# Performance work log

Measured on AMD Instinct MI355X. Metric: run time of the kernel, lower is better.

The kernel has to match this reference:

```python
import jax, jax.numpy as jnp
import numpy as np

N_HEAD = 8


def _axial_attn(x, wq, wk, wv, fw, fb, axis):
    # x: (B, T, H, W, C); axis is the axial axis in (B, nh, T, H, W, d): 2=T, 3=H, 4=W
    B, T, H, W, C = x.shape
    d = C // N_HEAD

    def heads(y):
        # (B,T,H,W,C) -> (B, nh, T, H, W, d)
        return jnp.moveaxis(y.reshape(B, T, H, W, N_HEAD, d), -2, 1)

    q, k, v = heads(x @ wq), heads(x @ wk), heads(x @ wv)
    # restrict attention to the axial axis: move it to -2, all other dims are batch
    q = jnp.moveaxis(q, axis, -2)
    k = jnp.moveaxis(k, axis, -2)
    v = jnp.moveaxis(v, axis, -2)
    scale = 1.0 / jnp.sqrt(jnp.asarray(d, x.dtype))
    scores = jnp.einsum('...ld,...md->...lm', q * scale, k)
    att = jax.nn.softmax(scores, axis=-1)
    o = jnp.einsum('...lm,...md->...ld', att, v)
    o = jnp.moveaxis(o, -2, axis)            # restore axial axis position
    o = jnp.moveaxis(o, 1, -2).reshape(B, T, H, W, C)  # merge heads
    return o @ fw + fb


def setup_inputs() -> dict:
    key = jax.random.key(0)
    ks = jax.random.split(key, 16)
    C = 512
    x = jax.random.normal(ks[0], (4, C, 16, 32, 32), jnp.float32)
    s = 0.02

    def w(k):
        return jax.random.normal(k, (C, C), jnp.float32) * s

    inp = {'x': x}
    i = 1
    for ax in ('w', 'h', 't'):
        inp[f'wq_{ax}'] = w(ks[i])
        inp[f'wk_{ax}'] = w(ks[i + 1])
        inp[f'wv_{ax}'] = w(ks[i + 2])
        inp[f'fc_{ax}'] = w(ks[i + 3])
        inp[f'fb_{ax}'] = jnp.zeros((C,), jnp.float32)
        i += 4
    return inp


def reference(x, wq_w, wk_w, wv_w, fc_w, fb_w,
              wq_h, wk_h, wv_h, fc_h, fb_h,
              wq_t, wk_t, wv_t, fc_t, fb_t):
    xt = jnp.moveaxis(x, 1, -1)  # (B, C, T, H, W) -> (B, T, H, W, C)
    out = (_axial_attn(xt, wq_w, wk_w, wv_w, fc_w, fb_w, 4)   # attend along W
           + _axial_attn(xt, wq_h, wk_h, wv_h, fc_h, fb_h, 3)  # attend along H
           + _axial_attn(xt, wq_t, wk_t, wv_t, fc_t, fb_t, 2))  # attend along T
    return jnp.moveaxis(out, -1, 1)  # back to (B, C, T, H, W)
```

## Files before the change

kernel.cpp:

```cpp
#include <hip/hip_runtime.h>
#include <stdint.h>

typedef __attribute__((ext_vector_type(8))) short bf16x8;
typedef __attribute__((ext_vector_type(4))) float f32x4;

static __device__ __forceinline__ short f2bf(float f) {
  uint32_t u = __builtin_bit_cast(uint32_t, f);
  u += 0x7fffu + ((u >> 16) & 1u);
  return (short)(u >> 16);
}

static __device__ __forceinline__ void gload_lds16(const void* g, void* l) {
  __builtin_amdgcn_global_load_lds((const __attribute__((address_space(1))) void*)g,
                                   (__attribute__((address_space(3))) void*)l, 16, 0, 0);
}

#define GFENCE asm volatile("" ::: "memory")

__global__ __launch_bounds__(256) void transpose_x_k(const float* __restrict__ x,
                                                     short* __restrict__ xb) {
  __shared__ float t[64][65];
  const int pt = blockIdx.x, ct = blockIdx.y, b = blockIdx.z;
  const int tid = threadIdx.x;
#pragma unroll
  for (int i = 0; i < 16; i++) {
    int cc = i * 4 + (tid >> 6);
    int pp = tid & 63;
    t[cc][pp] = x[(size_t)(b * 512 + ct * 64 + cc) * 16384 + pt * 64 + pp];
  }
  __syncthreads();
#pragma unroll
  for (int i = 0; i < 2; i++) {
    int seg = i * 256 + tid;
    int pw = seg >> 3, c8 = seg & 7;
    short tmp[8];
#pragma unroll
    for (int k = 0; k < 8; k++) tmp[k] = f2bf(t[c8 * 8 + k][pw]);
    *(uint4*)&xb[(size_t)(b * 16384 + pt * 64 + pw) * 512 + ct * 64 + c8 * 8] =
        *(const uint4*)tmp;
  }
}

struct WPtrs {
  const float* src[12];
  short* dst[12];
  int ld[12];
};

__global__ __launch_bounds__(256) void transpose_w_k(WPtrs P) {
  __shared__ float t[64][65];
  const int kt = blockIdx.x, nt = blockIdx.y, z = blockIdx.z;
  const float* src = P.src[z];
  short* dst = P.dst[z];
  const int ld = P.ld[z];
  const int tid = threadIdx.x;
#pragma unroll
  for (int i = 0; i < 16; i++) {
    int kk = i * 4 + (tid >> 6);
    int nn = tid & 63;
    t[kk][nn] = src[(kt * 64 + kk) * 512 + nt * 64 + nn];
  }
  __syncthreads();
#pragma unroll
  for (int i = 0; i < 2; i++) {
    int seg = i * 256 + tid;
    int nn = seg >> 3, k8 = seg & 7;
    short tmp[8];
#pragma unroll
    for (int k = 0; k < 8; k++) tmp[k] = f2bf(t[k8 * 8 + k][nn]);
    *(uint4*)&dst[(size_t)(nt * 64 + nn) * ld + kt * 64 + k8 * 8] = *(const uint4*)tmp;
  }
}

__global__ void bsum_k(const float* a, const float* b, const float* c, float* o) {
  int i = blockIdx.x * 256 + threadIdx.x;
  if (i < 512) o[i] = a[i] + b[i] + c[i];
}

#define LOADB(b, kh)                                                           \
  do {                                                                         \
    _Pragma("unroll") for (int ni = 0; ni < 4; ++ni) bfr[ni] =                 \
        *(const bf16x8*)(smem + ((b) * 4 + 2 + (kh)) * 16384 + boff +          \
                         ni * 1024);                                           \
  } while (0)

#define LOADA(b, kh, mq)                                                       \
  do {                                                                         \
    _Pragma("unroll") for (int mi = 0; mi < 4; ++mi) af[mi] =                  \
        *(const bf16x8*)(smem + ((b) * 4 + (kh)) * 16384 + aoff +              \
                         ((mq) * 4 + mi) * 1024);                              \
  } while (0)

#define MFMA16(mq)                                                             \
  do {                                                                         \
    __builtin_amdgcn_s_setprio(1);                                             \
    _Pragma("unroll") for (int mi = 0; mi < 4; ++mi)                           \
        _Pragma("unroll") for (int ni = 0; ni < 4; ++ni) acc[(mq) * 4 + mi]    \
            [ni] = __builtin_amdgcn_mfma_f32_16x16x32_bf16(                    \
                af[mi], bfr[ni], acc[(mq) * 4 + mi][ni], 0, 0, 0);             \
    __builtin_amdgcn_s_setprio(0);                                             \
    GFENCE;                                                                    \
  } while (0)

#define TILE(b, W0, W2, S0, S1, S2, S3)                                        \
  do {                                                                         \
    asm volatile("s_waitcnt vmcnt(" W0 ")" ::: "memory");                      \
    __builtin_amdgcn_s_barrier();                                              \
    GFENCE;                                                                    \
    LOADB(b, 0);                                                               \
    LOADA(b, 0, 0);                                                            \
    S0;                                                                        \
    MFMA16(0);                                                                 \
    __builtin_amdgcn_s_barrier();                                              \
    GFENCE;                                                                    \
    LOADA(b, 0, 1);                                                            \
    S1;                                                                        \
    MFMA16(1);                                                                 \
    asm volatile("s_waitcnt vmcnt(" W2 ")" ::: "memory");                      \
    __builtin_amdgcn_s_barrier();                                              \
    GFENCE;                                                                    \
    LOADB(b, 1);                                                               \
    LOADA(b, 1, 0);                                                            \
    S2;                                                                        \
    MFMA16(0);                                                                 \
    __builtin_amdgcn_s_barrier();                                              \
    GFENCE;                                                                    \
    LOADA(b, 1, 1);                                                            \
    S3;                                                                        \
    MFMA16(1);                                                                 \
  } while (0)

template <int MODE>
__global__ __launch_bounds__(512, 2) void gemm256_k(const short* __restrict__ A,
                                                    int lda,
                                                    const short* __restrict__ B,
                                                    int ldb, void* __restrict__ Dp,
                                                    int K, int ldd,
                                                    const float* __restrict__ bsum,
                                                    int GN) {
  extern __shared__ char smem[];
  const int tid = threadIdx.x;
  const int lane = tid & 63, wave = tid >> 6;
  const int wr = wave >> 2, wc = wave & 3;
  const int r4 = lane & 15, kl = lane >> 4;

  int bid = blockIdx.x;
  const int cpx = gridDim.x >> 3;
  bid = (bid & 7) * cpx + (bid >> 3);
  int bm, bn;
  if constexpr (MODE == 0) {
    bn = bid % GN;
    bm = bid / GN;
  } else {
    bm = bid & 1;
    bn = bid >> 1;
  }

  const int NT = K >> 6;

  const int srow = tid >> 2;
  const int schk = (tid & 3) ^ ((tid >> 4) & 3);
  const short* gA0 = A + (size_t)(bm * 256 + srow) * lda + schk * 8;
  const short* gB0 = B + (size_t)(bn * 256 + srow) * ldb + schk * 8;

  auto stage = [&](int tt, int x) {
    const short* g = (x < 2) ? gA0 : gB0;
    const size_t rstep = (size_t)128 * ((x < 2) ? lda : ldb);
    const size_t koff = (size_t)tt * 64 + (x & 1) * 32;
    char* ldst = smem + (((tt & 1) * 4 + x) * 16384) + wave * 1024;
#pragma unroll
    for (int i = 0; i < 2; ++i)
      gload_lds16(g + i * rstep + koff, ldst + i * 8192);
  };

  const int kls = kl ^ (r4 >> 2);
  const int aoff = wr * 8192 + r4 * 64 + kls * 16;
  const int boff = wc * 4096 + r4 * 64 + kls * 16;

  f32x4 acc[8][4];
#pragma unroll
  for (int i = 0; i < 8; ++i)
#pragma unroll
    for (int j = 0; j < 4; ++j) acc[i][j] = (f32x4){0.f, 0.f, 0.f, 0.f};
  bf16x8 af[4], bfr[4];

  stage(0, 0);
  stage(0, 2);
  stage(0, 1);
  stage(0, 3);
  stage(1, 0);
  stage(1, 2);

  int t = 0;
  for (; t < NT - 2; ++t) {
    const int b = t & 1;
    TILE(b, "8", "8", stage(t + 1, 1), stage(t + 1, 3), stage(t + 2, 0),
         stage(t + 2, 2));
  }
  {
    const int b = t & 1;
    TILE(b, "8", "8", stage(t + 1, 1), stage(t + 1, 3), (void)0, (void)0);
    ++t;
  }
  {
    const int b = t & 1;
    TILE(b, "4", "0", (void)0, (void)0, (void)0, (void)0);
  }

  const int m0 = wr * 128 + kl * 4;
  const int n0 = wc * 64 + r4;
  if (MODE == 0) {
    short* D = (short*)Dp;
#pragma unroll
    for (int mi = 0; mi < 8; ++mi)
#pragma unroll
      for (int ni = 0; ni < 4; ++ni)
#pragma unroll
        for (int r = 0; r < 4; ++r) {
          int row = bm * 256 + m0 + mi * 16 + r;
          int col = bn * 256 + n0 + ni * 16;
          D[(size_t)row * ldd + col] = f2bf(acc[mi][ni][r]);
        }
  } else {
    float* D = (float*)Dp + (size_t)((bn * 256) >> 14) * 8388608;
#pragma unroll
    for (int mi = 0; mi < 8; ++mi)
#pragma unroll
      for (int ni = 0; ni < 4; ++ni)
#pragma unroll
        for (int r = 0; r < 4; ++r) {
          int c = bm * 256 + m0 + mi * 16 + r;
          int n = (bn * 256 + n0 + ni * 16) & 16383;
          if (MODE == 1)
            D[(size_t)c * 16384 + n] = acc[mi][ni][r] + bsum[c];
          else
            D[(size_t)c * 16384 + n] += acc[mi][ni][r];
        }
  }
}

template <int L>
__global__ __launch_bounds__(256) void attn_mfma_k(const short* __restrict__ qkv,
                                                   short* __restrict__ o, int Adiv,
                                                   int Bmul, int Cmul, int stride,
                                                   int obase) {
  constexpr int MT = L / 16;
  constexpr int PITCH = 40;
  __shared__ short lds[4 * (32 + 64) * PITCH];
  const int tid = threadIdx.x;
  const int lane = tid & 63, wave = tid >> 6;
  short* p_lds = lds + wave * (96 * PITCH);
  short* vt = p_lds + 32 * PITCH;

  const int wid = blockIdx.x * 4 + wave;
  const int s = wid >> 3, head = wid & 7;
  const int base = (s / Adiv) * Bmul + (s % Adiv) * Cmul;
  const int r4 = lane & 15, kl = lane >> 4;

  if constexpr (L == 16) {
    for (int i = lane; i < 96 * PITCH; i += 64) p_lds[i] = 0;
  }

  bf16x8 qf[MT][2], kf[MT][2];
#pragma unroll
  for (int mi = 0; mi < MT; ++mi)
#pragma unroll
    for (int ks = 0; ks < 2; ++ks) {
      size_t nrow = (size_t)(base + (mi * 16 + r4) * stride) * 1536 + head * 64 +
                    ks * 32 + kl * 8;
      qf[mi][ks] = *(const bf16x8*)&qkv[nrow];
      kf[mi][ks] = *(const bf16x8*)&qkv[nrow + 512];
    }

#pragma unroll
  for (int it = 0; it < L / 8; ++it) {
    int j = (lane >> 3) + it * 8;
    uint4 u = *(const uint4*)&qkv[(size_t)(base + j * stride) * 1536 + 1024 +
                                  head * 64 + (lane & 7) * 8];
    ushort e[8];
    *(uint4*)e = u;
#pragma unroll
    for (int q = 0; q < 8; ++q) vt[((lane & 7) * 8 + q) * PITCH + j] = (short)e[q];
  }

  f32x4 sacc[MT][MT];
#pragma unroll
  for (int i = 0; i < MT; ++i)
#pragma unroll
    for (int j = 0; j < MT; ++j) sacc[i][j] = (f32x4){0.f, 0.f, 0.f, 0.f};
#pragma unroll
  for (int mi = 0; mi < MT; ++mi)
#pragma unroll
    for (int ni = 0; ni < MT; ++ni)
#pragma unroll
      for (int ks = 0; ks < 2; ++ks)
        sacc[mi][ni] = __builtin_amdgcn_mfma_f32_16x16x32_bf16(
            qf[mi][ks], kf[ni][ks], sacc[mi][ni], 0, 0, 0);

#pragma unroll
  for (int mi = 0; mi < MT; ++mi) {
    float mx[4], sm[4];
#pragma unroll
    for (int r = 0; r < 4; ++r) {
      float m = sacc[mi][0][r];
      if (MT == 2) m = fmaxf(m, sacc[mi][1][r]);
#pragma unroll
      for (int d = 1; d < 16; d <<= 1) m = fmaxf(m, __shfl_xor(m, d));
      mx[r] = m;
    }
#pragma unroll
    for (int ni = 0; ni < MT; ++ni)
#pragma unroll
      for (int r = 0; r < 4; ++r)
        sacc[mi][ni][r] = __expf((sacc[mi][ni][r] - mx[r]) * 0.125f);
#pragma unroll
    for (int r = 0; r < 4; ++r) {
      float t = sacc[mi][0][r];
      if (MT == 2) t += sacc[mi][1][r];
#pragma unroll
      for (int d = 1; d < 16; d <<= 1) t += __shfl_xor(t, d);
      sm[r] = 1.0f / t;
    }
#pragma unroll
    for (int ni = 0; ni < MT; ++ni)
#pragma unroll
      for (int r = 0; r < 4; ++r)
        p_lds[(mi * 16 + kl * 4 + r) * PITCH + ni * 16 + r4] =
            f2bf(sacc[mi][ni][r] * sm[r]);
  }
  asm volatile("s_waitcnt lgkmcnt(0)" ::: "memory");

  bf16x8 paf[MT], vbf[4];
#pragma unroll
  for (int mi = 0; mi < MT; ++mi)
    paf[mi] = *(const bf16x8*)&p_lds[(mi * 16 + r4) * PITCH + kl * 8];
#pragma unroll
  for (int nd = 0; nd < 4; ++nd)
    vbf[nd] = *(const bf16x8*)&vt[(nd * 16 + r4) * PITCH + kl * 8];
  f32x4 oacc[MT][4];
#pragma unroll
  for (int i = 0; i < MT; ++i)
#pragma unroll
    for (int j = 0; j < 4; ++j) oacc[i][j] = (f32x4){0.f, 0.f, 0.f, 0.f};
#pragma unroll
  for (int mi = 0; mi < MT; ++mi)
#pragma unroll
    for (int nd = 0; nd < 4; ++nd)
      oacc[mi][nd] = __builtin_amdgcn_mfma_f32_16x16x32_bf16(paf[mi], vbf[nd],
                                                             oacc[mi][nd], 0, 0, 0);

#pragma unroll
  for (int mi = 0; mi < MT; ++mi)
#pragma unroll
    for (int r = 0; r < 4; ++r) {
      int n = base + (mi * 16 + kl * 4 + r) * stride;
      size_t ob = (size_t)n * 1536 + obase + head * 64 + r4;
#pragma unroll
      for (int nd = 0; nd < 4; ++nd) o[ob + nd * 16] = f2bf(oacc[mi][nd][r]);
    }
}

extern "C" void kernel_launch(void* const* d_in, const int* in_sizes, int n_in,
                              void* d_out, int out_size, void* d_ws, size_t ws_size,
                              hipStream_t stream) {
  const float* x = (const float*)d_in[0];
  const float* wq[3];
  const float* wk[3];
  const float* wv[3];
  const float* fc[3];
  const float* fb[3];
  for (int a = 0; a < 3; a++) {
    wq[a] = (const float*)d_in[1 + a * 5];
    wk[a] = (const float*)d_in[2 + a * 5];
    wv[a] = (const float*)d_in[3 + a * 5];
    fc[a] = (const float*)d_in[4 + a * 5];
    fb[a] = (const float*)d_in[5 + a * 5];
  }
  char* ws = (char*)d_ws;
  short* xb = (short*)(ws);
  short* qkv = (short*)(ws + 67108864);
  short* wqkvt = (short*)(ws + 268435456);
  short* fctA = (short*)(ws + 273154048);
  float* bsum = (float*)(ws + 274726912);
  short* ob = (short*)(ws + 274728960);
  float* out = (float*)d_out;

  (void)hipFuncSetAttribute((const void*)&gemm256_k<0>,
                            hipFuncAttributeMaxDynamicSharedMemorySize, 131072);
  (void)hipFuncSetAttribute((const void*)&gemm256_k<1>,
                            hipFuncAttributeMaxDynamicSharedMemorySize, 131072);

  WPtrs P;
  for (int a = 0; a < 3; a++) {
    P.src[a * 4 + 0] = wq[a];
    P.src[a * 4 + 1] = wk[a];
    P.src[a * 4 + 2] = wv[a];
    P.src[a * 4 + 3] = fc[a];
    P.dst[a * 4 + 0] = wqkvt + (size_t)a * 1536 * 512;
    P.dst[a * 4 + 1] = wqkvt + (size_t)a * 1536 * 512 + 512 * 512;
    P.dst[a * 4 + 2] = wqkvt + (size_t)a * 1536 * 512 + 2 * 512 * 512;
    P.dst[a * 4 + 3] = fctA + a * 512;
    P.ld[a * 4 + 0] = 512;
    P.ld[a * 4 + 1] = 512;
    P.ld[a * 4 + 2] = 512;
    P.ld[a * 4 + 3] = 1536;
  }
  transpose_w_k<<<dim3(8, 8, 12), 256, 0, stream>>>(P);
  bsum_k<<<dim3(2), 256, 0, stream>>>(fb[0], fb[1], fb[2], bsum);
  transpose_x_k<<<dim3(256, 8, 4), 256, 0, stream>>>(x, xb);

  const int Ad[3] = {1, 32, 1024};
  const int Bm_[3] = {32, 1024, 16384};
  const int Cm[3] = {0, 1, 1};
  const int St[3] = {1, 32, 1024};
  const int Ls[3] = {32, 32, 16};

  for (int a = 0; a < 3; a++) {
    gemm256_k<0><<<dim3(1536), 512, 131072, stream>>>(
        xb, 512, wqkvt + (size_t)a * 1536 * 512, 512, (void*)qkv, 512, 1536,
        nullptr, 6);
    if (Ls[a] == 32)
      attn_mfma_k<32><<<dim3(4096), 256, 0, stream>>>(qkv, ob, Ad[a], Bm_[a], Cm[a],
                                                      St[a], a * 512);
    else
      attn_mfma_k<16><<<dim3(8192), 256, 0, stream>>>(qkv, ob, Ad[a], Bm_[a], Cm[a],
                                                      St[a], a * 512);
  }
  gemm256_k<1><<<dim3(512), 512, 131072, stream>>>(
      fctA, 1536, ob, 1536, (void*)out, 1536, 0, bsum, 0);
}
```

Baseline: 705.4 us.

## Double-buffer GEMM register fragments to prefetch LDS reads ahead of MFMAs

Rewrites the 256x256 bf16 GEMM main loop so the A/B fragments are held in two register sets. The LDS reads for the next quarter-tile, and for the next K tile's first fragments, are issued before the current MFMA batch runs. The aim is to hide LDS read latency behind matrix math, with vmcnt waits moved to fit the new order. This raises register pressure under the 512-thread, 2-blocks launch bound. The epilogue also drops the MODE 2 accumulate path, which changes results if that mode is still called.

After: 697.0 us. No clear change (-1.2%).

```diff
diff --git a/kernel.cpp b/kernel.cpp
--- a/kernel.cpp
+++ b/kernel.cpp
@@ -77,57 +77,64 @@
   if (i < 512) o[i] = a[i] + b[i] + c[i];
 }
 
-#define LOADB(b, kh)                                                           \
+#define READ_B(DST, b, kh)                                                     \
   do {                                                                         \
-    _Pragma("unroll") for (int ni = 0; ni < 4; ++ni) bfr[ni] =                 \
+    _Pragma("unroll") for (int ni = 0; ni < 4; ++ni) DST[ni] =                 \
         *(const bf16x8*)(smem + ((b) * 4 + 2 + (kh)) * 16384 + boff +          \
                          ni * 1024);                                           \
   } while (0)
 
-#define LOADA(b, kh, mq)                                                       \
+#define READ_A(DST, b, kh, mq)                                                 \
   do {                                                                         \
-    _Pragma("unroll") for (int mi = 0; mi < 4; ++mi) af[mi] =                  \
+    _Pragma("unroll") for (int mi = 0; mi < 4; ++mi) DST[mi] =                 \
         *(const bf16x8*)(smem + ((b) * 4 + (kh)) * 16384 + aoff +              \
                          ((mq) * 4 + mi) * 1024);                              \
   } while (0)
 
-#define MFMA16(mq)                                                             \
+#define MFMAX(mq, AF, BF)                                                      \
   do {                                                                         \
     __builtin_amdgcn_s_setprio(1);                                             \
     _Pragma("unroll") for (int mi = 0; mi < 4; ++mi)                           \
         _Pragma("unroll") for (int ni = 0; ni < 4; ++ni) acc[(mq) * 4 + mi]    \
             [ni] = __builtin_amdgcn_mfma_f32_16x16x32_bf16(                    \
-                af[mi], bfr[ni], acc[(mq) * 4 + mi][ni], 0, 0, 0);             \
+                AF[mi], BF[ni], acc[(mq) * 4 + mi][ni], 0, 0, 0);              \
     __builtin_amdgcn_s_setprio(0);                                             \
     GFENCE;                                                                    \
   } while (0)
 
-#define TILE(b, W0, W2, S0, S1, S2, S3)                                        \
+#define TILE_RA(b, b2, W1, W3, S0, S1, S2, S3, RA)                             \
   do {                                                                         \
-    asm volatile("s_waitcnt vmcnt(" W0 ")" ::: "memory");                      \
+                            \
     __builtin_amdgcn_s_barrier();                                              \
     GFENCE;                                                                    \
-    LOADB(b, 0);                                                               \
-    LOADA(b, 0, 0);                                                            \
+    READ_A(afB, b, 0, 1);                                                      \
     S0;                                                                        \
-    MFMA16(0);                                                                 \
+    GFENCE;                                                                    \
+    MFMAX(0, afA, bfA);                                                        \
+                     \
+    asm volatile("s_waitcnt vmcnt(" W1 ")" ::: "memory");                      \
     __builtin_amdgcn_s_barrier();                                              \
     GFENCE;                                                                    \
-    LOADA(b, 0, 1);                                                            \
+    READ_B(bfB, b, 1);                                                         \
+    READ_A(afA, b, 1, 0);                                                      \
     S1;                                                                        \
-    MFMA16(1);                                                                 \
-    asm volatile("s_waitcnt vmcnt(" W2 ")" ::: "memory");                      \
+    GFENCE;                                                                    \
+    MFMAX(1, afB, bfA);                                                        \
+                            \
     __builtin_amdgcn_s_barrier();                                              \
     GFENCE;                                                                    \
-    LOADB(b, 1);                                                               \
-    LOADA(b, 1, 0);                                                            \
+    READ_A(afB, b, 1, 1);                                                      \
     S2;                                                                        \
-    MFMA16(0);                                                                 \
+    GFENCE;                                                                    \
+    MFMAX(0, afA, bfB);                                                        \
+                 \
+    asm volatile("s_waitcnt vmcnt(" W3 ")" ::: "memory");                      \
     __builtin_amdgcn_s_barrier();                                              \
     GFENCE;                                                                    \
-    LOADA(b, 1, 1);                                                            \
+    RA;                                                                        \
     S3;                                                                        \
-    MFMA16(1);                                                                 \
+    GFENCE;                                                                    \
+    MFMAX(1, afB, bfB);                                                        \
   } while (0)
 
 template <int MODE>
@@ -182,7 +189,7 @@
   for (int i = 0; i < 8; ++i)
 #pragma unroll
     for (int j = 0; j < 4; ++j) acc[i][j] = (f32x4){0.f, 0.f, 0.f, 0.f};
-  bf16x8 af[4], bfr[4];
+  bf16x8 afA[4], afB[4], bfA[4], bfB[4];
 
   stage(0, 0);
   stage(0, 2);
@@ -190,21 +197,33 @@
   stage(0, 3);
   stage(1, 0);
   stage(1, 2);
+  asm volatile("s_waitcnt vmcnt(8)" ::: "memory");
+  __builtin_amdgcn_s_barrier();
+  GFENCE;
+  READ_B(bfA, 0, 0);
+  READ_A(afA, 0, 0, 0);
+  GFENCE;
 
   int t = 0;
   for (; t < NT - 2; ++t) {
-    const int b = t & 1;
-    TILE(b, "8", "8", stage(t + 1, 1), stage(t + 1, 3), stage(t + 2, 0),
-         stage(t + 2, 2));
+    const int b = t & 1, b2 = b ^ 1;
+    TILE_RA(b, b2, "6", "6", stage(t + 1, 1), stage(t + 1, 3), stage(t + 2, 0),
+            stage(t + 2, 2), {
+              READ_B(bfA, b2, 0);
+              READ_A(afA, b2, 0, 0);
+            });
   }
   {
-    const int b = t & 1;
-    TILE(b, "8", "8", stage(t + 1, 1), stage(t + 1, 3), (void)0, (void)0);
+    const int b = t & 1, b2 = b ^ 1;
+    TILE_RA(b, b2, "6", "4", stage(t + 1, 1), stage(t + 1, 3), (void)0, (void)0, {
+      READ_B(bfA, b2, 0);
+      READ_A(afA, b2, 0, 0);
+    });
     ++t;
   }
   {
-    const int b = t & 1;
-    TILE(b, "4", "0", (void)0, (void)0, (void)0, (void)0);
+    const int b = t & 1, b2 = b ^ 1;
+    TILE_RA(b, b2, "0", "0", (void)0, (void)0, (void)0, (void)0, (void)0);
   }
 
   const int m0 = wr * 128 + kl * 4;
@@ -231,10 +250,7 @@
         for (int r = 0; r < 4; ++r) {
           int c = bm * 256 + m0 + mi * 16 + r;
           int n = (bn * 256 + n0 + ni * 16) & 16383;
-          if (MODE == 1)
-            D[(size_t)c * 16384 + n] = acc[mi][ni][r] + bsum[c];
-          else
-            D[(size_t)c * 16384 + n] += acc[mi][ni][r];
+          D[(size_t)c * 16384 + n] = acc[mi][ni][r] + bsum[c];
         }
   }
 }
```

## Run 256x256 GEMM with 16 waves per block, one load per stage

Applied to the files above, without the earlier changes.

The GEMM block grows from 512 to 1024 threads, so each of 16 waves owns a 64x64 output sub-tile instead of 128x64. Per-thread accumulators halve and each stage issues a single global-to-LDS load per thread. The four-phase tile schedule with in-between barriers becomes two phases per k-tile, with adjusted vmcnt waits. This trades register pressure and per-wave MFMA work for more waves to hide latency, but adds barrier cost across 16 waves and lowers MFMA-to-LDS-read reuse per wave.

Measured after the change: 735.8 us. +4.3%, slower.

```diff
diff --git a/kernel.cpp b/kernel.cpp
--- a/kernel.cpp
+++ b/kernel.cpp
@@ -77,67 +77,46 @@
   if (i < 512) o[i] = a[i] + b[i] + c[i];
 }
 
-#define LOADB(b, kh)                                                           \
+#define READ_AB(b, kh)                                                         \
   do {                                                                         \
     _Pragma("unroll") for (int ni = 0; ni < 4; ++ni) bfr[ni] =                 \
         *(const bf16x8*)(smem + ((b) * 4 + 2 + (kh)) * 16384 + boff +          \
                          ni * 1024);                                           \
+    _Pragma("unroll") for (int mi = 0; mi < 4; ++mi) af[mi] =                  \
+        *(const bf16x8*)(smem + ((b) * 4 + (kh)) * 16384 + aoff + mi * 1024);  \
   } while (0)
 
-#define LOADA(b, kh, mq)                                                       \
-  do {                                                                         \
-    _Pragma("unroll") for (int mi = 0; mi < 4; ++mi) af[mi] =                  \
-        *(const bf16x8*)(smem + ((b) * 4 + (kh)) * 16384 + aoff +              \
-                         ((mq) * 4 + mi) * 1024);                              \
-  } while (0)
-
-#define MFMA16(mq)                                                             \
+#define MFMA16X                                                                \
   do {                                                                         \
     __builtin_amdgcn_s_setprio(1);                                             \
     _Pragma("unroll") for (int mi = 0; mi < 4; ++mi)                           \
-        _Pragma("unroll") for (int ni = 0; ni < 4; ++ni) acc[(mq) * 4 + mi]    \
-            [ni] = __builtin_amdgcn_mfma_f32_16x16x32_bf16(                    \
-                af[mi], bfr[ni], acc[(mq) * 4 + mi][ni], 0, 0, 0);             \
+        _Pragma("unroll") for (int ni = 0; ni < 4; ++ni) acc[mi][ni] =         \
+            __builtin_amdgcn_mfma_f32_16x16x32_bf16(af[mi], bfr[ni],           \
+                                                    acc[mi][ni], 0, 0, 0);     \
     __builtin_amdgcn_s_setprio(0);                                             \
     GFENCE;                                                                    \
   } while (0)
 
-#define TILE(b, W0, W2, S0, S1, S2, S3)                                        \
+#define PH(b, kh, W, SA, SB)                                                   \
   do {                                                                         \
-    asm volatile("s_waitcnt vmcnt(" W0 ")" ::: "memory");                      \
+    asm volatile("s_waitcnt vmcnt(" W ")" ::: "memory");                       \
     __builtin_amdgcn_s_barrier();                                              \
     GFENCE;                                                                    \
-    LOADB(b, 0);                                                               \
-    LOADA(b, 0, 0);                                                            \
-    S0;                                                                        \
-    MFMA16(0);                                                                 \
-    __builtin_amdgcn_s_barrier();                                              \
+    READ_AB(b, kh);                                                            \
+    SA;                                                                        \
+    SB;                                                                        \
     GFENCE;                                                                    \
-    LOADA(b, 0, 1);                                                            \
-    S1;                                                                        \
-    MFMA16(1);                                                                 \
-    asm volatile("s_waitcnt vmcnt(" W2 ")" ::: "memory");                      \
-    __builtin_amdgcn_s_barrier();                                              \
-    GFENCE;                                                                    \
-    LOADB(b, 1);                                                               \
-    LOADA(b, 1, 0);                                                            \
-    S2;                                                                        \
-    MFMA16(0);                                                                 \
-    __builtin_amdgcn_s_barrier();                                              \
-    GFENCE;                                                                    \
-    LOADA(b, 1, 1);                                                            \
-    S3;                                                                        \
-    MFMA16(1);                                                                 \
+    MFMA16X;                                                                   \
   } while (0)
 
 template <int MODE>
-__global__ __launch_bounds__(512, 2) void gemm256_k(const short* __restrict__ A,
-                                                    int lda,
-                                                    const short* __restrict__ B,
-                                                    int ldb, void* __restrict__ Dp,
-                                                    int K, int ldd,
-                                                    const float* __restrict__ bsum,
-                                                    int GN) {
+__global__ __launch_bounds__(1024) void gemm256_k(const short* __restrict__ A,
+                                                  int lda,
+                                                  const short* __restrict__ B,
+                                                  int ldb, void* __restrict__ Dp,
+                                                  int K, int ldd,
+                                                  const float* __restrict__ bsum,
+                                                  int GN) {
   extern __shared__ char smem[];
   const int tid = threadIdx.x;
   const int lane = tid & 63, wave = tid >> 6;
@@ -165,21 +144,17 @@
 
   auto stage = [&](int tt, int x) {
     const short* g = (x < 2) ? gA0 : gB0;
-    const size_t rstep = (size_t)128 * ((x < 2) ? lda : ldb);
     const size_t koff = (size_t)tt * 64 + (x & 1) * 32;
-    char* ldst = smem + (((tt & 1) * 4 + x) * 16384) + wave * 1024;
-#pragma unroll
-    for (int i = 0; i < 2; ++i)
-      gload_lds16(g + i * rstep + koff, ldst + i * 8192);
+    gload_lds16(g + koff, smem + (((tt & 1) * 4 + x) * 16384) + wave * 1024);
   };
 
   const int kls = kl ^ (r4 >> 2);
-  const int aoff = wr * 8192 + r4 * 64 + kls * 16;
+  const int aoff = wr * 4096 + r4 * 64 + kls * 16;
   const int boff = wc * 4096 + r4 * 64 + kls * 16;
 
-  f32x4 acc[8][4];
-#pragma unroll
-  for (int i = 0; i < 8; ++i)
+  f32x4 acc[4][4];
+#pragma unroll
+  for (int i = 0; i < 4; ++i)
 #pragma unroll
     for (int j = 0; j < 4; ++j) acc[i][j] = (f32x4){0.f, 0.f, 0.f, 0.f};
   bf16x8 af[4], bfr[4];
@@ -194,25 +169,27 @@
   int t = 0;
   for (; t < NT - 2; ++t) {
     const int b = t & 1;
-    TILE(b, "8", "8", stage(t + 1, 1), stage(t + 1, 3), stage(t + 2, 0),
-         stage(t + 2, 2));
+    PH(b, 0, "4", stage(t + 1, 1), stage(t + 1, 3));
+    PH(b, 1, "4", stage(t + 2, 0), stage(t + 2, 2));
   }
   {
     const int b = t & 1;
-    TILE(b, "8", "8", stage(t + 1, 1), stage(t + 1, 3), (void)0, (void)0);
+    PH(b, 0, "4", stage(t + 1, 1), stage(t + 1, 3));
+    PH(b, 1, "4", (void)0, (void)0);
     ++t;
   }
   {
     const int b = t & 1;
-    TILE(b, "4", "0", (void)0, (void)0, (void)0, (void)0);
-  }
-
-  const int m0 = wr * 128 + kl * 4;
+    PH(b, 0, "2", (void)0, (void)0);
+    PH(b, 1, "0", (void)0, (void)0);
+  }
+
+  const int m0 = wr * 64 + kl * 4;
   const int n0 = wc * 64 + r4;
   if (MODE == 0) {
     short* D = (short*)Dp;
 #pragma unroll
-    for (int mi = 0; mi < 8; ++mi)
+    for (int mi = 0; mi < 4; ++mi)
 #pragma unroll
       for (int ni = 0; ni < 4; ++ni)
 #pragma unroll
@@ -224,17 +201,14 @@
   } else {
     float* D = (float*)Dp + (size_t)((bn * 256) >> 14) * 8388608;
 #pragma unroll
-    for (int mi = 0; mi < 8; ++mi)
+    for (int mi = 0; mi < 4; ++mi)
 #pragma unroll
       for (int ni = 0; ni < 4; ++ni)
 #pragma unroll
         for (int r = 0; r < 4; ++r) {
           int c = bm * 256 + m0 + mi * 16 + r;
           int n = (bn * 256 + n0 + ni * 16) & 16383;
-          if (MODE == 1)
-            D[(size_t)c * 16384 + n] = acc[mi][ni][r] + bsum[c];
-          else
-            D[(size_t)c * 16384 + n] += acc[mi][ni][r];
+          D[(size_t)c * 16384 + n] = acc[mi][ni][r] + bsum[c];
         }
   }
 }
@@ -416,7 +390,7 @@
   const int Ls[3] = {32, 32, 16};
 
   for (int a = 0; a < 3; a++) {
-    gemm256_k<0><<<dim3(1536), 512, 131072, stream>>>(
+    gemm256_k<0><<<dim3(1536), 1024, 131072, stream>>>(
         xb, 512, wqkvt + (size_t)a * 1536 * 512, 512, (void*)qkv, 512, 1536,
         nullptr, 6);
     if (Ls[a] == 32)
@@ -426,6 +400,6 @@
       attn_mfma_k<16><<<dim3(8192), 256, 0, stream>>>(qkv, ob, Ad[a], Bm_[a], Cm[a],
                                                       St[a], a * 512);
   }
-  gemm256_k<1><<<dim3(512), 512, 131072, stream>>>(
+  gemm256_k<1><<<dim3(512), 1024, 131072, stream>>>(
       fctA, 1536, ob, 1536, (void*)out, 1536, 0, bsum, 0);
 }
```
